# Kernel tuning notes

Measured on AMD Instinct MI355X. Metric: run time of the kernel, lower is better.

## Reference

```python
import math
import jax, jax.numpy as jnp
import numpy as np

ALPHA = 0.2                         # LeakyReLU slope
LAMBDA_INIT = 0.8 - 0.6 * math.exp(-0.3 * 1)  # lambda_init_fn(depth=1)
NEG_INF = -9e15
EPS_LN = 1e-5

B, N, IN_F, OUT_F = 4, 2048, 512, 512
INTERNAL = OUT_F // 2
REL_DIM = 10
NUM_REL = 6


def setup_inputs() -> dict:
    key = jax.random.key(0)
    ks = jax.random.split(key, 16)
    xav = lambda k, shape, fan: jax.random.normal(k, shape, jnp.float32) * (1.414 * math.sqrt(2.0 / fan))
    h = jax.random.normal(ks[0], (B, N, IN_F), jnp.float32)
    adj = jax.random.randint(ks[1], (B, N, N), 0, NUM_REL, jnp.int32)
    W = xav(ks[2], (IN_F, OUT_F), IN_F + OUT_F)
    a_left_pos = xav(ks[3], (INTERNAL,), INTERNAL + 1)
    a_right_pos = xav(ks[4], (INTERNAL,), INTERNAL + 1)
    a_left_neg = xav(ks[5], (INTERNAL,), INTERNAL + 1)
    a_right_neg = xav(ks[6], (INTERNAL,), INTERNAL + 1)
    rel_table = jax.random.normal(ks[7], (NUM_REL, REL_DIM), jnp.float32)
    a_rel_pos = xav(ks[8], (REL_DIM,), REL_DIM + 1)
    a_rel_neg = xav(ks[9], (REL_DIM,), REL_DIM + 1)
    ll1 = 0.1 * jax.random.normal(ks[10], (INTERNAL,), jnp.float32)
    lr1 = 0.1 * jax.random.normal(ks[11], (INTERNAL,), jnp.float32)
    ll2 = 0.1 * jax.random.normal(ks[12], (INTERNAL,), jnp.float32)
    lr2 = 0.1 * jax.random.normal(ks[13], (INTERNAL,), jnp.float32)
    ln_gamma = jnp.ones((OUT_F,), jnp.float32)
    ln_beta = jnp.zeros((OUT_F,), jnp.float32)
    return dict(h=h, adj=adj, W=W, a_left_pos=a_left_pos, a_right_pos=a_right_pos,
                a_left_neg=a_left_neg, a_right_neg=a_right_neg, rel_table=rel_table,
                a_rel_pos=a_rel_pos, a_rel_neg=a_rel_neg, ll1=ll1, lr1=lr1,
                ll2=ll2, lr2=lr2, ln_gamma=ln_gamma, ln_beta=ln_beta)


def _leaky(x):
    return jnp.where(x >= 0, x, ALPHA * x)


def reference(h, adj, W, a_left_pos, a_right_pos, a_left_neg, a_right_neg,
              rel_table, a_rel_pos, a_rel_neg, ll1, lr1, ll2, lr2,
              ln_gamma, ln_beta):
    # Projection: Wh [B,N,out] -> split into pos/neg halves [B,N,internal]
    Wh = jnp.einsum('bni,io->bno', h, W)
    Bn, Nn, _ = Wh.shape
    Wh2 = Wh.reshape(Bn, Nn, 2, INTERNAL)
    Wh_pos, Wh_neg = Wh2[:, :, 0, :], Wh2[:, :, 1, :]

    # Additive GAT-style scores: e[b,i,j] = a_left.Wh[i] + a_right.Wh[j]
    e_pos = (Wh_pos @ a_left_pos)[:, :, None] + (Wh_pos @ a_right_pos)[:, None, :]
    e_neg = (Wh_neg @ a_left_neg)[:, :, None] + (Wh_neg @ a_right_neg)[:, None, :]

    # Relation-embedding bias: gather [B,N,N,rel_dim] then project to scalar
    rel_emb = rel_table[adj]                       # [B,N,N,R]
    e_pos = e_pos + rel_emb @ a_rel_pos
    e_neg = e_neg + rel_emb @ a_rel_neg

    mask = adj > 0
    att_pos = jax.nn.softmax(jnp.where(mask, _leaky(e_pos), NEG_INF), axis=2)
    att_neg = jax.nn.softmax(jnp.where(mask, _leaky(e_neg), NEG_INF), axis=2)

    lam = jnp.exp(jnp.sum(ll1 * lr1)) - jnp.exp(jnp.sum(ll2 * lr2)) + LAMBDA_INIT
    attention = att_pos - lam * att_neg            # dropout is identity (eval)

    Wh_v = jnp.concatenate([Wh_pos, Wh_neg], axis=-1)   # [B,N,out]
    h_prime = jnp.einsum('bij,bjd->bid', attention, Wh_v)

    mu = jnp.mean(h_prime, axis=-1, keepdims=True)
    var = jnp.mean(jnp.square(h_prime - mu), axis=-1, keepdims=True)
    h_prime = (h_prime - mu) / jnp.sqrt(var + EPS_LN) * ln_gamma + ln_beta
    h_prime = h_prime * (1 - LAMBDA_INIT)
    return jax.nn.gelu(h_prime, approximate=False), attention
```

## Files before the change

### kernel.cpp

```cpp
#include <hip/hip_runtime.h>
#include <hip/hip_bf16.h>


#define B_ 4
#define N_ 2048
#define F_ 512
#define ALPHA_ 0.2f
#define NEG_INF_ -9000000000000000.0f
#define EPS_LN_ 1e-5f

typedef __attribute__((ext_vector_type(8))) short bf16x8;
typedef __attribute__((ext_vector_type(4))) short bf16x4;
typedef __attribute__((ext_vector_type(4))) float f32x4;

#define HBF_OFF   0
#define WT_OFF    8388608
#define EL_OFF    8912896
#define HP_OFF    0
#define WHT_OFF   16777216
#define ATTBF_OFF 25165824
#define CANON_OFF 58720256
#define SC_OFF    58732864
#define FLAG_OFF  58732928
#define V_OFF     58736640

#define C_ALP 0
#define C_ARP 256
#define C_ALN 512
#define C_ARN 768
#define C_GAM 2128
#define C_BET 2640

__device__ __forceinline__ float bf_as_f32(unsigned short u) {
    return __uint_as_float(((unsigned)u) << 16);
}
__device__ __forceinline__ float ldf(const void* p, long i, int isf32) {
    return isf32 ? ((const float*)p)[i] : bf_as_f32(((const unsigned short*)p)[i]);
}
__device__ __forceinline__ short f2bf(float f) {
    __hip_bfloat16 t = __float2bfloat16(f);
    return *reinterpret_cast<short*>(&t);
}

#define GLL16(g, l) __builtin_amdgcn_global_load_lds( \
    (const __attribute__((address_space(1))) void*)(g), \
    (__attribute__((address_space(3))) void*)(l), 16, 0, 0)

__global__ void k_prep(const unsigned short* __restrict__ hraw,
                       const void* alp, const void* arp, const void* aln, const void* arn,
                       const void* rel, const void* arelp, const void* areln,
                       const void* ll1, const void* lr1, const void* ll2, const void* lr2,
                       const void* gam, const void* bet,
                       int* __restrict__ flag, float* __restrict__ canon, float* __restrict__ sc,
                       float* __restrict__ v) {
    __shared__ float wmax[4];
    __shared__ int s_fl;
    int tid = threadIdx.x, lane = tid & 63, wid = tid >> 6;
    float mx = 0.f;
    for (int i = tid; i < 8192; i += 256) {
        float x = fabsf(bf_as_f32(hraw[i]));
        if (x == x && x > mx) mx = x;
    }
    for (int off = 32; off; off >>= 1) mx = fmaxf(mx, __shfl_down(mx, off));
    if (lane == 0) wmax[wid] = mx;
    __syncthreads();
    if (tid == 0) {
        float m = fmaxf(fmaxf(wmax[0], wmax[1]), fmaxf(wmax[2], wmax[3]));
        int f = (m > 1e10f) ? 1 : 0;
        s_fl = f; flag[0] = f;
    }
    __syncthreads();
    int fl = s_fl;
    for (int i = tid; i < 2048; i += 256) v[i] = 0.f;
    canon[C_ALP + tid] = ldf(alp, tid, fl);
    canon[C_ARP + tid] = ldf(arp, tid, fl);
    canon[C_ALN + tid] = ldf(aln, tid, fl);
    canon[C_ARN + tid] = ldf(arn, tid, fl);
    canon[C_GAM + tid] = ldf(gam, tid, fl);
    canon[C_GAM + 256 + tid] = ldf(gam, 256 + tid, fl);
    canon[C_BET + tid] = ldf(bet, tid, fl);
    canon[C_BET + 256 + tid] = ldf(bet, 256 + tid, fl);
    if (wid == 0) {
        float s1 = 0.f, s2 = 0.f;
        for (int k = lane; k < 256; k += 64) {
            s1 += ldf(ll1, k, fl) * ldf(lr1, k, fl);
            s2 += ldf(ll2, k, fl) * ldf(lr2, k, fl);
        }
        for (int off = 32; off; off >>= 1) { s1 += __shfl_down(s1, off); s2 += __shfl_down(s2, off); }
        if (lane == 0) {
            float lam_init = 0.8f - 0.6f * expf(-0.3f);
            sc[0] = expf(s1) - expf(s2) + lam_init;
        }
    } else if (wid == 1 && lane < 6) {
        float p = 0.f, n = 0.f;
        for (int d = 0; d < 10; ++d) {
            float rv = ldf(rel, lane * 10 + d, fl);
            p += rv * ldf(arelp, d, fl);
            n += rv * ldf(areln, d, fl);
        }
        sc[1 + lane] = p;
        sc[7 + lane] = n;
    }
}

__global__ __launch_bounds__(256) void k_transW(const void* __restrict__ W, const int* __restrict__ flag,
                                                __hip_bfloat16* __restrict__ Wt,
                                                const float* __restrict__ canon, float* __restrict__ v) {
    __shared__ float t[32][33];
    int fl = flag[0];
    int k0 = blockIdx.x * 32, o0 = blockIdx.y * 32;
    int tx = threadIdx.x & 31, ty = threadIdx.x >> 5;
#pragma unroll
    for (int r = 0; r < 4; ++r)
        t[ty + r * 8][tx] = ldf(W, (k0 + ty + r * 8) * 512 + o0 + tx, fl);
    __syncthreads();
#pragma unroll
    for (int r = 0; r < 4; ++r)
        Wt[(o0 + ty + r * 8) * 512 + k0 + tx] = __float2bfloat16(t[tx][ty + r * 8]);
    int kl = threadIdx.x >> 3;
    int seg = threadIdx.x & 7;
    int neg = o0 >= 256;
    const float* aL = canon + (neg ? C_ALN : C_ALP) + (o0 & 255);
    const float* aR = canon + (neg ? C_ARN : C_ARP) + (o0 & 255);
    float s0 = 0.f, s1 = 0.f;
#pragma unroll
    for (int e = 0; e < 4; ++e) {
        float w = t[kl][seg * 4 + e];
        s0 += w * aL[seg * 4 + e];
        s1 += w * aR[seg * 4 + e];
    }
    s0 += __shfl_xor(s0, 1); s0 += __shfl_xor(s0, 2); s0 += __shfl_xor(s0, 4);
    s1 += __shfl_xor(s1, 1); s1 += __shfl_xor(s1, 2); s1 += __shfl_xor(s1, 4);
    if (seg == 0) {
        int vb = neg ? 2 : 0;
        atomicAdd(&v[(vb + 0) * 512 + k0 + kl], s0);
        atomicAdd(&v[(vb + 1) * 512 + k0 + kl], s1);
    }
}

__global__ __launch_bounds__(256) void k_conv_h8(const void* __restrict__ h, const int* __restrict__ flag,
                                                 short* __restrict__ hbf, const float* __restrict__ v,
                                                 float* __restrict__ el) {
    int fl = flag[0];
    int tid = threadIdx.x, lane = tid & 63;
    long i = ((long)blockIdx.x * 256 + tid) * 8;
    int row = (int)(i >> 9);
    float f[8];
    if (fl) {
        const float4* p = (const float4*)((const float*)h + i);
        float4 a = p[0], b = p[1];
        f[0] = a.x; f[1] = a.y; f[2] = a.z; f[3] = a.w;
        f[4] = b.x; f[5] = b.y; f[6] = b.z; f[7] = b.w;
    } else {
        bf16x8 x = *(const bf16x8*)((const short*)h + i);
#pragma unroll
        for (int e = 0; e < 8; ++e) f[e] = bf_as_f32((unsigned short)x[e]);
    }
    bf16x8 vv;
#pragma unroll
    for (int e = 0; e < 8; ++e) vv[e] = f2bf(f[e]);
    *(bf16x8*)(hbf + i) = vv;
    const float* v0 = v + 0 * 512 + lane * 8;
    const float* v1 = v + 1 * 512 + lane * 8;
    const float* v2 = v + 2 * 512 + lane * 8;
    const float* v3 = v + 3 * 512 + lane * 8;
    float slp = 0.f, srp = 0.f, sln = 0.f, srn = 0.f;
#pragma unroll
    for (int e = 0; e < 8; ++e) {
        slp += f[e] * v0[e]; srp += f[e] * v1[e];
        sln += f[e] * v2[e]; srn += f[e] * v3[e];
    }
    for (int off = 32; off; off >>= 1) {
        slp += __shfl_xor(slp, off); srp += __shfl_xor(srp, off);
        sln += __shfl_xor(sln, off); srn += __shfl_xor(srn, off);
    }
    if (lane == 0) {
        el[row] = slp; el[8192 + row] = srp; el[16384 + row] = sln; el[24576 + row] = srn;
    }
}

template<int TRANS_OUT>
__global__ __launch_bounds__(256) void k_gemm(const short* __restrict__ A, const short* __restrict__ B,
                                              void* __restrict__ Cout, int K, int N,
                                              long aBatch, long bBatch, long cBatch) {
    __shared__ short SM[12288];
    short* As = SM;
    short* Bs = SM + 8192;
    int tid = threadIdx.x, wid = tid >> 6, lane = tid & 63;
    int bm = blockIdx.x * 128, bn = blockIdx.y * 64, bz = blockIdx.z;
    const short* Ab = A + bz * aBatch + (long)bm * K;
    const short* Bb = B + bz * bBatch + (long)bn * K;
    f32x4 acc[4][2] = {};
    int wr = (wid >> 1) * 64, wc = (wid & 1) * 32;
    int l15 = lane & 15, lhi = lane >> 4;
    for (int k0 = 0; k0 < K; k0 += 64) {
        __syncthreads();
#pragma unroll
        for (int j = 0; j < 4; ++j) {
            int q = tid + j * 256;
            int row = q >> 3, c = (q & 7) ^ (row & 7);
            GLL16(Ab + (long)row * K + k0 + c * 8, As + q * 8);
        }
#pragma unroll
        for (int j = 0; j < 2; ++j) {
            int q = tid + j * 256;
            int row = q >> 3, c = (q & 7) ^ (row & 7);
            GLL16(Bb + (long)row * K + k0 + c * 8, Bs + q * 8);
        }
        __syncthreads();
#pragma unroll
        for (int ks = 0; ks < 2; ++ks) {
            bf16x8 af[4], bq[2];
#pragma unroll
            for (int m = 0; m < 4; ++m) {
                int r = wr + m * 16 + l15;
                int c = (ks * 4 + lhi) ^ (r & 7);
                af[m] = *(const bf16x8*)&As[r * 64 + c * 8];
            }
#pragma unroll
            for (int n = 0; n < 2; ++n) {
                int r = wc + n * 16 + l15;
                int c = (ks * 4 + lhi) ^ (r & 7);
                bq[n] = *(const bf16x8*)&Bs[r * 64 + c * 8];
            }
#pragma unroll
            for (int m = 0; m < 4; ++m)
#pragma unroll
                for (int n = 0; n < 2; ++n)
                    acc[m][n] = __builtin_amdgcn_mfma_f32_16x16x32_bf16(af[m], bq[n], acc[m][n], 0, 0, 0);
        }
    }
    int rg = lhi * 4;
    if (TRANS_OUT == 0) {
        float* C = (float*)Cout + bz * cBatch;
#pragma unroll
        for (int m = 0; m < 4; ++m)
#pragma unroll
            for (int n = 0; n < 2; ++n)
#pragma unroll
                for (int r = 0; r < 4; ++r)
                    C[(long)(bm + wr + m * 16 + rg + r) * N + bn + wc + n * 16 + l15] = acc[m][n][r];
    } else {
        __syncthreads();
        short* T = SM;
#pragma unroll
        for (int m = 0; m < 4; ++m)
#pragma unroll
            for (int n = 0; n < 2; ++n) {
                bf16x4 p;
#pragma unroll
                for (int r = 0; r < 4; ++r) p[r] = f2bf(acc[m][n][r]);
                int o = wc + n * 16 + l15;
                int jj = wr + m * 16 + rg;
                *(bf16x4*)&T[o * 136 + jj] = p;
            }
        __syncthreads();
        int b = bm >> 11, jb = bm & 2047;
        int o = tid >> 2, sg = tid & 3;
        short* Wg = (short*)Cout + ((long)b * 512 + bn + o) * 2048 + jb + sg * 32;
#pragma unroll
        for (int w2 = 0; w2 < 4; ++w2)
            *(bf16x8*)(Wg + w2 * 8) = *(bf16x8*)&T[o * 136 + sg * 32 + w2 * 8];
    }
}

__global__ __launch_bounds__(256) void k_attn(const int* __restrict__ adj,
                                              const float* __restrict__ el, const float* __restrict__ sc,
                                              float* __restrict__ att_f32,
                                              __hip_bfloat16* __restrict__ att_bf) {
    __shared__ float s_rp[8], s_rn[8], s_lam[1];
    __shared__ float rmp[4], rmn[4], rsp[4], rsn[4];
    int tid = threadIdx.x, lane = tid & 63, wid = tid >> 6;
    if (tid < 6) { s_rp[tid] = sc[1 + tid]; s_rn[tid] = sc[7 + tid]; }
    if (tid == 6) s_lam[0] = sc[0];
    int m = blockIdx.x, b = m >> 11;
    float elp = el[m], eln = el[16384 + m];
    const float* erp = el + 8192 + b * 2048;
    const float* ern = el + 24576 + b * 2048;
    const int* adjr = adj + (long)m * 2048;
    __syncthreads();
    int j0 = tid * 8;
    int4 A0 = *(const int4*)(adjr + j0), A1 = *(const int4*)(adjr + j0 + 4);
    float4 P0 = *(const float4*)(erp + j0), P1 = *(const float4*)(erp + j0 + 4);
    float4 Q0 = *(const float4*)(ern + j0), Q1 = *(const float4*)(ern + j0 + 4);
    int aa[8] = {A0.x, A0.y, A0.z, A0.w, A1.x, A1.y, A1.z, A1.w};
    float rp[8] = {P0.x, P0.y, P0.z, P0.w, P1.x, P1.y, P1.z, P1.w};
    float rn[8] = {Q0.x, Q0.y, Q0.z, Q0.w, Q1.x, Q1.y, Q1.z, Q1.w};
    float sp[8], sn[8];
    float mp = NEG_INF_, mn = NEG_INF_;
#pragma unroll
    for (int e = 0; e < 8; ++e) {
        int a = aa[e];
        float ep = elp + rp[e] + s_rp[a];
        float en = eln + rn[e] + s_rn[a];
        ep = ep >= 0.f ? ep : ALPHA_ * ep;
        en = en >= 0.f ? en : ALPHA_ * en;
        sp[e] = a > 0 ? ep : NEG_INF_;
        sn[e] = a > 0 ? en : NEG_INF_;
        mp = fmaxf(mp, sp[e]); mn = fmaxf(mn, sn[e]);
    }
    for (int off = 32; off; off >>= 1) { mp = fmaxf(mp, __shfl_down(mp, off)); mn = fmaxf(mn, __shfl_down(mn, off)); }
    if (lane == 0) { rmp[wid] = mp; rmn[wid] = mn; }
    __syncthreads();
    mp = fmaxf(fmaxf(rmp[0], rmp[1]), fmaxf(rmp[2], rmp[3]));
    mn = fmaxf(fmaxf(rmn[0], rmn[1]), fmaxf(rmn[2], rmn[3]));
    float sump = 0.f, sumn = 0.f;
#pragma unroll
    for (int e = 0; e < 8; ++e) {
        sp[e] = __expf(sp[e] - mp);
        sn[e] = __expf(sn[e] - mn);
        sump += sp[e]; sumn += sn[e];
    }
    for (int off = 32; off; off >>= 1) { sump += __shfl_down(sump, off); sumn += __shfl_down(sumn, off); }
    if (lane == 0) { rsp[wid] = sump; rsn[wid] = sumn; }
    __syncthreads();
    sump = rsp[0] + rsp[1] + rsp[2] + rsp[3];
    sumn = rsn[0] + rsn[1] + rsn[2] + rsn[3];
    float ip = 1.0f / sump, inn = 1.0f / sumn;
    float lam = s_lam[0];
    float vout[8];
    bf16x8 vb;
#pragma unroll
    for (int e = 0; e < 8; ++e) {
        vout[e] = sp[e] * ip - lam * sn[e] * inn;
        vb[e] = f2bf(vout[e]);
    }
    float* of = att_f32 + (long)m * 2048 + j0;
    *(float4*)(of)     = make_float4(vout[0], vout[1], vout[2], vout[3]);
    *(float4*)(of + 4) = make_float4(vout[4], vout[5], vout[6], vout[7]);
    *(bf16x8*)((short*)att_bf + (long)m * 2048 + j0) = vb;
}

__global__ __launch_bounds__(256) void k_lngelu(const float* __restrict__ HP, const float* __restrict__ canon,
                                                float* __restrict__ out) {
    int wid = threadIdx.x >> 6, lane = threadIdx.x & 63;
    int m = blockIdx.x * 4 + wid;
    const float* Hr = HP + (long)m * 512 + lane * 8;
    float4 x0 = *(const float4*)(Hr), x1 = *(const float4*)(Hr + 4);
    float x[8] = {x0.x, x0.y, x0.z, x0.w, x1.x, x1.y, x1.z, x1.w};
    float s = 0.f, ss = 0.f;
#pragma unroll
    for (int e = 0; e < 8; ++e) { s += x[e]; ss += x[e] * x[e]; }
    for (int off = 32; off; off >>= 1) { s += __shfl_xor(s, off); ss += __shfl_xor(ss, off); }
    float mu = s * (1.0f / 512.0f);
    float var = ss * (1.0f / 512.0f) - mu * mu;
    float inv = rsqrtf(fmaxf(var, 0.0f) + EPS_LN_);
    float scale = 1.0f - (0.8f - 0.6f * expf(-0.3f));
    const float* g8 = canon + C_GAM + lane * 8;
    const float* b8 = canon + C_BET + lane * 8;
    float o[8];
#pragma unroll
    for (int e = 0; e < 8; ++e) {
        float y = (x[e] - mu) * inv * g8[e] + b8[e];
        y *= scale;
        o[e] = 0.5f * y * (1.0f + erff(y * 0.70710678118654752f));
    }
    float* op = out + (long)m * 512 + lane * 8;
    *(float4*)(op)     = make_float4(o[0], o[1], o[2], o[3]);
    *(float4*)(op + 4) = make_float4(o[4], o[5], o[6], o[7]);
}

extern "C" void kernel_launch(void* const* d_in, const int* in_sizes, int n_in,
                              void* d_out, int out_size, void* d_ws, size_t ws_size,
                              hipStream_t stream) {
    const void* h   = d_in[0];
    const int*  adj = (const int*)d_in[1];
    const void* W   = d_in[2];

    char* ws = (char*)d_ws;
    short*          hbf   = (short*)(ws + HBF_OFF);
    __hip_bfloat16* Wt    = (__hip_bfloat16*)(ws + WT_OFF);
    float*          el    = (float*)(ws + EL_OFF);
    float*          HP    = (float*)(ws + HP_OFF);
    __hip_bfloat16* Wht   = (__hip_bfloat16*)(ws + WHT_OFF);
    __hip_bfloat16* attbf = (__hip_bfloat16*)(ws + ATTBF_OFF);
    float*          can   = (float*)(ws + CANON_OFF);
    float*          sc    = (float*)(ws + SC_OFF);
    int*            flg   = (int*)(ws + FLAG_OFF);
    float*          v     = (float*)(ws + V_OFF);

    float* out_gelu = (float*)d_out;
    float* out_att  = out_gelu + (size_t)B_ * N_ * F_;

    k_prep<<<1, 256, 0, stream>>>((const unsigned short*)h,
                                  d_in[3], d_in[4], d_in[5], d_in[6], d_in[7], d_in[8], d_in[9],
                                  d_in[10], d_in[11], d_in[12], d_in[13], d_in[14], d_in[15],
                                  flg, can, sc, v);
    k_transW<<<dim3(16, 16), 256, 0, stream>>>(W, flg, Wt, can, v);
    k_conv_h8<<<2048, 256, 0, stream>>>(h, flg, hbf, v, el);
    k_gemm<1><<<dim3(64, 8, 1), 256, 0, stream>>>(hbf, (const short*)Wt, Wht, 512, 512, 0, 0, 0);
    k_attn<<<8192, 256, 0, stream>>>(adj, el, sc, out_att, attbf);
    k_gemm<0><<<dim3(16, 8, 4), 256, 0, stream>>>((const short*)attbf, (const short*)Wht, HP, 2048, 512,
                                                  2048L * 2048, 512L * 2048, 2048L * 512);
    k_lngelu<<<2048, 256, 0, stream>>>(HP, can, out_gelu);
}
```

Baseline: 276.2 us.

## Merge prep kernels into one launch and double GEMM K-tile depth

Replaces the single-block prep kernel and the W-transpose kernel with one multi-role kernel. Each block now detects the input dtype locally from a 64-element sample instead of reading a global flag, and the attention-vector projections are computed directly without atomics. This removes one launch and the serial dependency on the one-block prep kernel. Separately, the GEMM K tile grows from 64 to 128 (doubling LDS use), halving the loop's barrier count, at the cost of lower occupancy. Sampling only 64 elements for dtype detection is less robust than the previous 8192-element scan.

New measurement: 267.8 us. -3.0%, faster.

```diff
diff --git a/kernel.cpp b/kernel.cpp
--- a/kernel.cpp
+++ b/kernel.cpp
@@ -20,16 +20,8 @@
 #define WHT_OFF   16777216
 #define ATTBF_OFF 25165824
 #define CANON_OFF 58720256
-#define SC_OFF    58732864
-#define FLAG_OFF  58732928
-#define V_OFF     58736640
-
-#define C_ALP 0
-#define C_ARP 256
-#define C_ALN 512
-#define C_ARN 768
-#define C_GAM 2128
-#define C_BET 2640
+#define SC_OFF    58724352
+#define V_OFF     58724416
 
 __device__ __forceinline__ float bf_as_f32(unsigned short u) {
     return __uint_as_float(((unsigned)u) << 16);
@@ -41,107 +33,91 @@
     __hip_bfloat16 t = __float2bfloat16(f);
     return *reinterpret_cast<short*>(&t);
 }
+__device__ __forceinline__ int detect_f32(const unsigned short* p) {
+    float mx = 0.f;
+    for (int i = 0; i < 64; ++i) {
+        float x = fabsf(bf_as_f32(p[i]));
+        if (x == x && x > mx) mx = x;
+    }
+    return mx > 1e10f;
+}
 
 #define GLL16(g, l) __builtin_amdgcn_global_load_lds( \
     (const __attribute__((address_space(1))) void*)(g), \
     (__attribute__((address_space(3))) void*)(l), 16, 0, 0)
 
-__global__ void k_prep(const unsigned short* __restrict__ hraw,
-                       const void* alp, const void* arp, const void* aln, const void* arn,
-                       const void* rel, const void* arelp, const void* areln,
-                       const void* ll1, const void* lr1, const void* ll2, const void* lr2,
-                       const void* gam, const void* bet,
-                       int* __restrict__ flag, float* __restrict__ canon, float* __restrict__ sc,
-                       float* __restrict__ v) {
-    __shared__ float wmax[4];
-    __shared__ int s_fl;
-    int tid = threadIdx.x, lane = tid & 63, wid = tid >> 6;
-    float mx = 0.f;
-    for (int i = tid; i < 8192; i += 256) {
-        float x = fabsf(bf_as_f32(hraw[i]));
-        if (x == x && x > mx) mx = x;
-    }
-    for (int off = 32; off; off >>= 1) mx = fmaxf(mx, __shfl_down(mx, off));
-    if (lane == 0) wmax[wid] = mx;
-    __syncthreads();
-    if (tid == 0) {
-        float m = fmaxf(fmaxf(wmax[0], wmax[1]), fmaxf(wmax[2], wmax[3]));
-        int f = (m > 1e10f) ? 1 : 0;
-        s_fl = f; flag[0] = f;
-    }
-    __syncthreads();
-    int fl = s_fl;
-    for (int i = tid; i < 2048; i += 256) v[i] = 0.f;
-    canon[C_ALP + tid] = ldf(alp, tid, fl);
-    canon[C_ARP + tid] = ldf(arp, tid, fl);
-    canon[C_ALN + tid] = ldf(aln, tid, fl);
-    canon[C_ARN + tid] = ldf(arn, tid, fl);
-    canon[C_GAM + tid] = ldf(gam, tid, fl);
-    canon[C_GAM + 256 + tid] = ldf(gam, 256 + tid, fl);
-    canon[C_BET + tid] = ldf(bet, tid, fl);
-    canon[C_BET + 256 + tid] = ldf(bet, 256 + tid, fl);
-    if (wid == 0) {
-        float s1 = 0.f, s2 = 0.f;
-        for (int k = lane; k < 256; k += 64) {
-            s1 += ldf(ll1, k, fl) * ldf(lr1, k, fl);
-            s2 += ldf(ll2, k, fl) * ldf(lr2, k, fl);
-        }
-        for (int off = 32; off; off >>= 1) { s1 += __shfl_down(s1, off); s2 += __shfl_down(s2, off); }
-        if (lane == 0) {
-            float lam_init = 0.8f - 0.6f * expf(-0.3f);
-            sc[0] = expf(s1) - expf(s2) + lam_init;
-        }
-    } else if (wid == 1 && lane < 6) {
-        float p = 0.f, n = 0.f;
-        for (int d = 0; d < 10; ++d) {
-            float rv = ldf(rel, lane * 10 + d, fl);
-            p += rv * ldf(arelp, d, fl);
-            n += rv * ldf(areln, d, fl);
-        }
-        sc[1 + lane] = p;
-        sc[7 + lane] = n;
-    }
-}
-
-__global__ __launch_bounds__(256) void k_transW(const void* __restrict__ W, const int* __restrict__ flag,
-                                                __hip_bfloat16* __restrict__ Wt,
-                                                const float* __restrict__ canon, float* __restrict__ v) {
+__global__ __launch_bounds__(256) void k_pre(const unsigned short* __restrict__ hraw, const void* __restrict__ W,
+                                             const void* alp, const void* arp, const void* aln, const void* arn,
+                                             const void* rel, const void* arelp, const void* areln,
+                                             const void* ll1, const void* lr1, const void* ll2, const void* lr2,
+                                             const void* gam, const void* bet,
+                                             __hip_bfloat16* __restrict__ Wt, float* __restrict__ v,
+                                             float* __restrict__ canon, float* __restrict__ sc) {
     __shared__ float t[32][33];
-    int fl = flag[0];
-    int k0 = blockIdx.x * 32, o0 = blockIdx.y * 32;
-    int tx = threadIdx.x & 31, ty = threadIdx.x >> 5;
-#pragma unroll
-    for (int r = 0; r < 4; ++r)
-        t[ty + r * 8][tx] = ldf(W, (k0 + ty + r * 8) * 512 + o0 + tx, fl);
-    __syncthreads();
-#pragma unroll
-    for (int r = 0; r < 4; ++r)
-        Wt[(o0 + ty + r * 8) * 512 + k0 + tx] = __float2bfloat16(t[tx][ty + r * 8]);
-    int kl = threadIdx.x >> 3;
-    int seg = threadIdx.x & 7;
-    int neg = o0 >= 256;
-    const float* aL = canon + (neg ? C_ALN : C_ALP) + (o0 & 255);
-    const float* aR = canon + (neg ? C_ARN : C_ARP) + (o0 & 255);
-    float s0 = 0.f, s1 = 0.f;
-#pragma unroll
-    for (int e = 0; e < 4; ++e) {
-        float w = t[kl][seg * 4 + e];
-        s0 += w * aL[seg * 4 + e];
-        s1 += w * aR[seg * 4 + e];
-    }
-    s0 += __shfl_xor(s0, 1); s0 += __shfl_xor(s0, 2); s0 += __shfl_xor(s0, 4);
-    s1 += __shfl_xor(s1, 1); s1 += __shfl_xor(s1, 2); s1 += __shfl_xor(s1, 4);
-    if (seg == 0) {
-        int vb = neg ? 2 : 0;
-        atomicAdd(&v[(vb + 0) * 512 + k0 + kl], s0);
-        atomicAdd(&v[(vb + 1) * 512 + k0 + kl], s1);
-    }
-}
-
-__global__ __launch_bounds__(256) void k_conv_h8(const void* __restrict__ h, const int* __restrict__ flag,
-                                                 short* __restrict__ hbf, const float* __restrict__ v,
-                                                 float* __restrict__ el) {
-    int fl = flag[0];
+    int fl = detect_f32(hraw);
+    int bi = blockIdx.x, tid = threadIdx.x, lane = tid & 63, wid = tid >> 6;
+    if (bi < 256) {
+        int k0 = (bi & 15) * 32, o0 = (bi >> 4) * 32;
+        int tx = tid & 31, ty = tid >> 5;
+#pragma unroll
+        for (int r = 0; r < 4; ++r)
+            t[ty + r * 8][tx] = ldf(W, (long)(k0 + ty + r * 8) * 512 + o0 + tx, fl);
+        __syncthreads();
+#pragma unroll
+        for (int r = 0; r < 4; ++r)
+            Wt[(o0 + ty + r * 8) * 512 + k0 + tx] = __float2bfloat16(t[tx][ty + r * 8]);
+    } else if (bi < 272) {
+        int k = (bi - 256) * 32 + (tid >> 3);
+        int seg = tid & 7;
+        int pos = seg < 4;
+        int ob = (seg & 3) * 64 + (pos ? 0 : 256);
+        const void* aL = pos ? alp : aln;
+        const void* aR = pos ? arp : arn;
+        float sL = 0.f, sR = 0.f;
+        for (int e = 0; e < 64; ++e) {
+            float w = ldf(W, (long)k * 512 + ob + e, fl);
+            sL += w * ldf(aL, (ob & 255) + e, fl);
+            sR += w * ldf(aR, (ob & 255) + e, fl);
+        }
+        sL += __shfl_xor(sL, 1); sL += __shfl_xor(sL, 2);
+        sR += __shfl_xor(sR, 1); sR += __shfl_xor(sR, 2);
+        if ((seg & 3) == 0) {
+            int vb = pos ? 0 : 2;
+            v[vb * 512 + k] = sL;
+            v[(vb + 1) * 512 + k] = sR;
+        }
+    } else {
+        canon[tid] = ldf(gam, tid, fl);
+        canon[256 + tid] = ldf(gam, 256 + tid, fl);
+        canon[512 + tid] = ldf(bet, tid, fl);
+        canon[768 + tid] = ldf(bet, 256 + tid, fl);
+        if (wid == 0) {
+            float s1 = 0.f, s2 = 0.f;
+            for (int k = lane; k < 256; k += 64) {
+                s1 += ldf(ll1, k, fl) * ldf(lr1, k, fl);
+                s2 += ldf(ll2, k, fl) * ldf(lr2, k, fl);
+            }
+            for (int off = 32; off; off >>= 1) { s1 += __shfl_down(s1, off); s2 += __shfl_down(s2, off); }
+            if (lane == 0) {
+                float lam_init = 0.8f - 0.6f * expf(-0.3f);
+                sc[0] = expf(s1) - expf(s2) + lam_init;
+            }
+        } else if (wid == 1 && lane < 6) {
+            float p = 0.f, n = 0.f;
+            for (int d = 0; d < 10; ++d) {
+                float rv = ldf(rel, lane * 10 + d, fl);
+                p += rv * ldf(arelp, d, fl);
+                n += rv * ldf(areln, d, fl);
+            }
+            sc[1 + lane] = p;
+            sc[7 + lane] = n;
+        }
+    }
+}
+
+__global__ __launch_bounds__(256) void k_conv(const void* __restrict__ h, short* __restrict__ hbf,
+                                              const float* __restrict__ v, float* __restrict__ el) {
+    int fl = detect_f32((const unsigned short*)h);
     int tid = threadIdx.x, lane = tid & 63;
     long i = ((long)blockIdx.x * 256 + tid) * 8;
     int row = (int)(i >> 9);
@@ -183,9 +159,9 @@
 __global__ __launch_bounds__(256) void k_gemm(const short* __restrict__ A, const short* __restrict__ B,
                                               void* __restrict__ Cout, int K, int N,
                                               long aBatch, long bBatch, long cBatch) {
-    __shared__ short SM[12288];
+    __shared__ short SM[24576];
     short* As = SM;
-    short* Bs = SM + 8192;
+    short* Bs = SM + 16384;
     int tid = threadIdx.x, wid = tid >> 6, lane = tid & 63;
     int bm = blockIdx.x * 128, bn = blockIdx.y * 64, bz = blockIdx.z;
     const short* Ab = A + bz * aBatch + (long)bm * K;
@@ -193,35 +169,35 @@
     f32x4 acc[4][2] = {};
     int wr = (wid >> 1) * 64, wc = (wid & 1) * 32;
     int l15 = lane & 15, lhi = lane >> 4;
-    for (int k0 = 0; k0 < K; k0 += 64) {
-        __syncthreads();
+    for (int k0 = 0; k0 < K; k0 += 128) {
+        __syncthreads();
+#pragma unroll
+        for (int j = 0; j < 8; ++j) {
+            int q = tid + j * 256;
+            int row = q >> 4, c = (q & 15) ^ (row & 7);
+            GLL16(Ab + (long)row * K + k0 + c * 8, As + q * 8);
+        }
 #pragma unroll
         for (int j = 0; j < 4; ++j) {
             int q = tid + j * 256;
-            int row = q >> 3, c = (q & 7) ^ (row & 7);
-            GLL16(Ab + (long)row * K + k0 + c * 8, As + q * 8);
-        }
-#pragma unroll
-        for (int j = 0; j < 2; ++j) {
-            int q = tid + j * 256;
-            int row = q >> 3, c = (q & 7) ^ (row & 7);
+            int row = q >> 4, c = (q & 15) ^ (row & 7);
             GLL16(Bb + (long)row * K + k0 + c * 8, Bs + q * 8);
         }
         __syncthreads();
 #pragma unroll
-        for (int ks = 0; ks < 2; ++ks) {
+        for (int ks = 0; ks < 4; ++ks) {
             bf16x8 af[4], bq[2];
 #pragma unroll
             for (int m = 0; m < 4; ++m) {
                 int r = wr + m * 16 + l15;
                 int c = (ks * 4 + lhi) ^ (r & 7);
-                af[m] = *(const bf16x8*)&As[r * 64 + c * 8];
+                af[m] = *(const bf16x8*)&As[r * 128 + c * 8];
             }
 #pragma unroll
             for (int n = 0; n < 2; ++n) {
                 int r = wc + n * 16 + l15;
                 int c = (ks * 4 + lhi) ^ (r & 7);
-                bq[n] = *(const bf16x8*)&Bs[r * 64 + c * 8];
+                bq[n] = *(const bf16x8*)&Bs[r * 128 + c * 8];
             }
 #pragma unroll
             for (int m = 0; m < 4; ++m)
@@ -346,8 +322,8 @@
     float var = ss * (1.0f / 512.0f) - mu * mu;
     float inv = rsqrtf(fmaxf(var, 0.0f) + EPS_LN_);
     float scale = 1.0f - (0.8f - 0.6f * expf(-0.3f));
-    const float* g8 = canon + C_GAM + lane * 8;
-    const float* b8 = canon + C_BET + lane * 8;
+    const float* g8 = canon + lane * 8;
+    const float* b8 = canon + 512 + lane * 8;
     float o[8];
 #pragma unroll
     for (int e = 0; e < 8; ++e) {
@@ -376,18 +352,16 @@
     __hip_bfloat16* attbf = (__hip_bfloat16*)(ws + ATTBF_OFF);
     float*          can   = (float*)(ws + CANON_OFF);
     float*          sc    = (float*)(ws + SC_OFF);
-    int*            flg   = (int*)(ws + FLAG_OFF);
     float*          v     = (float*)(ws + V_OFF);
 
     float* out_gelu = (float*)d_out;
     float* out_att  = out_gelu + (size_t)B_ * N_ * F_;
 
-    k_prep<<<1, 256, 0, stream>>>((const unsigned short*)h,
-                                  d_in[3], d_in[4], d_in[5], d_in[6], d_in[7], d_in[8], d_in[9],
-                                  d_in[10], d_in[11], d_in[12], d_in[13], d_in[14], d_in[15],
-                                  flg, can, sc, v);
-    k_transW<<<dim3(16, 16), 256, 0, stream>>>(W, flg, Wt, can, v);
-    k_conv_h8<<<2048, 256, 0, stream>>>(h, flg, hbf, v, el);
+    k_pre<<<273, 256, 0, stream>>>((const unsigned short*)h, W,
+                                   d_in[3], d_in[4], d_in[5], d_in[6], d_in[7], d_in[8], d_in[9],
+                                   d_in[10], d_in[11], d_in[12], d_in[13], d_in[14], d_in[15],
+                                   Wt, v, can, sc);
+    k_conv<<<2048, 256, 0, stream>>>(h, hbf, v, el);
     k_gemm<1><<<dim3(64, 8, 1), 256, 0, stream>>>(hbf, (const short*)Wt, Wht, 512, 512, 0, 0, 0);
     k_attn<<<8192, 256, 0, stream>>>(adj, el, sc, out_att, attbf);
     k_gemm<0><<<dim3(16, 8, 4), 256, 0, stream>>>((const short*)attbf, (const short*)Wht, HP, 2048, 512,
```
